# Kernel tuning notes

Measured on AMD Instinct MI355X. Metric: run time of the kernel, lower is better.

The kernel has to match this reference:

```python
import jax, jax.numpy as jnp
import numpy as np

B = 8192
IN = 1024
H = 1024


def setup_inputs() -> dict:
    key = jax.random.key(0)
    ks = jax.random.split(key, 7)
    stdv = 1.0 / np.sqrt(H)
    u = lambda k, shape: jax.random.uniform(k, shape, jnp.float32, -stdv, stdv)
    return {
        "input": jax.random.normal(ks[0], (B, IN), jnp.float32),
        "h_prev": jax.random.normal(ks[1], (B, H), jnp.float32),
        "c_prev": jax.random.normal(ks[2], (B, H), jnp.float32),
        "W_ih": u(ks[3], (4 * H, IN)),
        "b_ih": u(ks[4], (4 * H,)),
        "W_hh": u(ks[5], (4 * H, H)),
        "b_hh": u(ks[6], (4 * H,)),
    }


def reference(input, h_prev, c_prev, W_ih, b_ih, W_hh, b_hh):
    # gates: [B, 4H] = input @ W_ih^T + b_ih + h_prev @ W_hh^T + b_hh
    gates = (jnp.einsum("bi,gi->bg", input, W_ih) + b_ih
             + jnp.einsum("bh,gh->bg", h_prev, W_hh) + b_hh)
    i_in, f_in, g_in, o_in = jnp.split(gates, 4, axis=1)
    i_t = jax.nn.sigmoid(i_in)
    f_t = jax.nn.sigmoid(f_in)
    g_t = jnp.tanh(g_in)
    o_t = jax.nn.sigmoid(o_in)
    c_t = f_t * c_prev + i_t * g_t
    h_t = o_t * jnp.tanh(c_t)
    return (h_t, c_t)
```

## Files before the change

kernel.cpp:

```cpp
#include <hip/hip_runtime.h>
#include <hip/hip_bf16.h>
#include <stdint.h>


typedef __attribute__((ext_vector_type(8))) __bf16 bf16x8;
typedef __attribute__((ext_vector_type(8))) unsigned short u16x8;
typedef __attribute__((ext_vector_type(4))) float f32x4;

__device__ __forceinline__ unsigned short f2bf(float f) {
  union { float f; unsigned int u; } v; v.f = f;
  unsigned int u = v.u;
  unsigned int r = u + 0x7FFFu + ((u >> 16) & 1u);
  return (unsigned short)(r >> 16);
}

__global__ void cvt_kernel(const float* __restrict__ src,
                           unsigned short* __restrict__ dst, int n4) {
  int i = blockIdx.x * blockDim.x + threadIdx.x;
  int stride = gridDim.x * blockDim.x;
  for (; i < n4; i += stride) {
    float4 v = ((const float4*)src)[i];
    ushort4 o;
    o.x = f2bf(v.x); o.y = f2bf(v.y); o.z = f2bf(v.z); o.w = f2bf(v.w);
    ((ushort4*)dst)[i] = o;
  }
}

#define GLOAD_LDS(gp, lofs)                                                    \
  __builtin_amdgcn_global_load_lds(                                            \
      (const __attribute__((address_space(1))) void*)(gp),                     \
      (__attribute__((address_space(3))) void*)(smem_raw + (lofs)), 16, 0, 0)

__global__ void lstm_fused(const unsigned short* __restrict__ Xb,
                           const unsigned short* __restrict__ Hb,
                           const unsigned short* __restrict__ Wihb,
                           const unsigned short* __restrict__ Whhb,
                           const float* __restrict__ bih,
                           const float* __restrict__ bhh,
                           const float* __restrict__ cprev,
                           float* __restrict__ out) {
  __shared__ __align__(16) char smem_raw[32768];
  unsigned short (*sA)[64] = (unsigned short (*)[64])smem_raw;
  unsigned short (*sB)[64] = (unsigned short (*)[64])(smem_raw + 16384);
  float (*eps)[128] = (float (*)[128])smem_raw;

  const int tid = threadIdx.x;
  const int lane = tid & 63;
  const int wid = tid >> 6;
  const int wr = wid >> 1;
  const int wc = wid & 1;
  const int l15 = lane & 15;
  const int l4 = lane >> 4;

  const int m0 = blockIdx.x * 128;
  const int h0 = blockIdx.y * 32;

  const int srow = tid >> 3;
  const int scol = (tid & 7) << 3;

  f32x4 acc[4][4];
#pragma unroll
  for (int m = 0; m < 4; ++m)
#pragma unroll
    for (int n = 0; n < 4; ++n) {
      f32x4 z = {0.f, 0.f, 0.f, 0.f};
      acc[m][n] = z;
    }

  for (int k0 = 0; k0 < 2048; k0 += 64) {
    const unsigned short* As = (k0 < 1024) ? Xb : Hb;
    const unsigned short* Bs = (k0 < 1024) ? Wihb : Whhb;
    const int kk = k0 & 1023;
#pragma unroll
    for (int p = 0; p < 4; ++p) {
      const unsigned short* ga =
          As + (size_t)(m0 + p * 32 + srow) * 1024 + kk + scol;
      GLOAD_LDS(ga, p * 4096 + wid * 1024);
      const unsigned short* gb =
          Bs + (size_t)(p * 1024 + h0 + srow) * 1024 + kk + scol;
      GLOAD_LDS(gb, 16384 + p * 4096 + wid * 1024);
    }
    __syncthreads();
#pragma unroll
    for (int kk2 = 0; kk2 < 2; ++kk2) {
      bf16x8 afr[4], bfr[4];
#pragma unroll
      for (int m = 0; m < 4; ++m) {
        u16x8 t = *(const u16x8*)&sA[wr * 64 + m * 16 + l15][kk2 * 32 + l4 * 8];
        afr[m] = __builtin_bit_cast(bf16x8, t);
      }
#pragma unroll
      for (int n = 0; n < 4; ++n) {
        u16x8 t = *(const u16x8*)&sB[wc * 64 + n * 16 + l15][kk2 * 32 + l4 * 8];
        bfr[n] = __builtin_bit_cast(bf16x8, t);
      }
#pragma unroll
      for (int m = 0; m < 4; ++m)
#pragma unroll
        for (int n = 0; n < 4; ++n)
          acc[m][n] = __builtin_amdgcn_mfma_f32_16x16x32_bf16(afr[m], bfr[n],
                                                              acc[m][n], 0, 0, 0);
    }
    __syncthreads();
  }

#pragma unroll
  for (int phase = 0; phase < 2; ++phase) {
    if (wr == phase) {
#pragma unroll
      for (int m = 0; m < 4; ++m)
#pragma unroll
        for (int n = 0; n < 4; ++n)
#pragma unroll
          for (int r = 0; r < 4; ++r)
            eps[m * 16 + l4 * 4 + r][wc * 64 + n * 16 + l15] = acc[m][n][r];
    }
    __syncthreads();
#pragma unroll
    for (int it = 0; it < 8; ++it) {
      int idx = it * 256 + tid;
      int h = idx & 31;
      int r = idx >> 5;
      int gh = h0 + h;
      size_t grow = (size_t)(m0 + phase * 64 + r);
      float vi = eps[r][h]       + bih[gh]         + bhh[gh];
      float vf = eps[r][32 + h]  + bih[1024 + gh]  + bhh[1024 + gh];
      float vg = eps[r][64 + h]  + bih[2048 + gh]  + bhh[2048 + gh];
      float vo = eps[r][96 + h]  + bih[3072 + gh]  + bhh[3072 + gh];
      float si = 1.f / (1.f + __expf(-vi));
      float sf = 1.f / (1.f + __expf(-vf));
      float tg = tanhf(vg);
      float so = 1.f / (1.f + __expf(-vo));
      float cp = cprev[grow * 1024 + gh];
      float ct = sf * cp + si * tg;
      float ht = so * tanhf(ct);
      out[grow * 1024 + gh] = ht;
      out[(size_t)8388608 + grow * 1024 + gh] = ct;
    }
    __syncthreads();
  }
}

extern "C" void kernel_launch(void* const* d_in, const int* in_sizes, int n_in,
                              void* d_out, int out_size, void* d_ws, size_t ws_size,
                              hipStream_t stream) {
  const float* input  = (const float*)d_in[0];
  const float* h_prev = (const float*)d_in[1];
  const float* c_prev = (const float*)d_in[2];
  const float* W_ih   = (const float*)d_in[3];
  const float* b_ih   = (const float*)d_in[4];
  const float* W_hh   = (const float*)d_in[5];
  const float* b_hh   = (const float*)d_in[6];
  float* out = (float*)d_out;

  unsigned short* Xb   = (unsigned short*)d_ws;
  unsigned short* Hb   = Xb + (size_t)8192 * 1024;
  unsigned short* Wihb = Hb + (size_t)8192 * 1024;
  unsigned short* Whhb = Wihb + (size_t)4096 * 1024;

  cvt_kernel<<<1024, 256, 0, stream>>>(input, Xb, 8192 * 1024 / 4);
  cvt_kernel<<<1024, 256, 0, stream>>>(h_prev, Hb, 8192 * 1024 / 4);
  cvt_kernel<<<512, 256, 0, stream>>>(W_ih, Wihb, 4096 * 1024 / 4);
  cvt_kernel<<<512, 256, 0, stream>>>(W_hh, Whhb, 4096 * 1024 / 4);

  dim3 grid(64, 32);
  lstm_fused<<<grid, 256, 0, stream>>>(Xb, Hb, Wihb, Whhb, b_ih, b_hh, c_prev, out);
}
```

Measured before the change: 346.8 us.

## Rewrite LSTM GEMM with 256x64 tiles, deep LDS pipeline, merged conversion kernel

Merges the four fp32-to-bf16 conversion launches into one 2D-grid kernel that writes 8 elements per thread. The fused GEMM is restructured to 512-thread blocks computing 256x(4x64) tiles. It uses a multi-stage global_load_lds ring buffer across 128KB LDS with explicit vmcnt waits, interleaved prefetch, setprio around MFMA bursts and a swizzled block-to-tile mapping. The epilogue is reorganized to read accumulators per lane from LDS. This aims to raise data reuse and hide memory latency, at the cost of heavy LDS use that limits occupancy, and it relies on fragile manual synchronization.

Result: no change. 353.0 us (+1.8%).

```diff
diff --git a/kernel.cpp b/kernel.cpp
--- a/kernel.cpp
+++ b/kernel.cpp
@@ -9,135 +9,176 @@
 
 __device__ __forceinline__ unsigned short f2bf(float f) {
   union { float f; unsigned int u; } v; v.f = f;
-  unsigned int u = v.u;
-  unsigned int r = u + 0x7FFFu + ((u >> 16) & 1u);
+  unsigned int r = v.u + 0x7FFFu + ((v.u >> 16) & 1u);
   return (unsigned short)(r >> 16);
 }
 
-__global__ void cvt_kernel(const float* __restrict__ src,
-                           unsigned short* __restrict__ dst, int n4) {
+__global__ void cvt_all(const float* __restrict__ s0, const float* __restrict__ s1,
+                        const float* __restrict__ s2, const float* __restrict__ s3,
+                        unsigned short* __restrict__ d0, unsigned short* __restrict__ d1,
+                        unsigned short* __restrict__ d2, unsigned short* __restrict__ d3) {
+  const float* src; unsigned short* dst; int n8;
+  if (blockIdx.y == 0)      { src = s0; dst = d0; n8 = 8192 * 128; }
+  else if (blockIdx.y == 1) { src = s1; dst = d1; n8 = 8192 * 128; }
+  else if (blockIdx.y == 2) { src = s2; dst = d2; n8 = 4096 * 128; }
+  else                      { src = s3; dst = d3; n8 = 4096 * 128; }
   int i = blockIdx.x * blockDim.x + threadIdx.x;
   int stride = gridDim.x * blockDim.x;
-  for (; i < n4; i += stride) {
-    float4 v = ((const float4*)src)[i];
-    ushort4 o;
-    o.x = f2bf(v.x); o.y = f2bf(v.y); o.z = f2bf(v.z); o.w = f2bf(v.w);
-    ((ushort4*)dst)[i] = o;
+  for (; i < n8; i += stride) {
+    float4 a = ((const float4*)src)[2 * i];
+    float4 b = ((const float4*)src)[2 * i + 1];
+    u16x8 o;
+    o[0] = f2bf(a.x); o[1] = f2bf(a.y); o[2] = f2bf(a.z); o[3] = f2bf(a.w);
+    o[4] = f2bf(b.x); o[5] = f2bf(b.y); o[6] = f2bf(b.z); o[7] = f2bf(b.w);
+    *(u16x8*)&dst[(size_t)i * 8] = o;
   }
 }
 
-#define GLOAD_LDS(gp, lofs)                                                    \
-  __builtin_amdgcn_global_load_lds(                                            \
-      (const __attribute__((address_space(1))) void*)(gp),                     \
-      (__attribute__((address_space(3))) void*)(smem_raw + (lofs)), 16, 0, 0)
-
-__global__ void lstm_fused(const unsigned short* __restrict__ Xb,
-                           const unsigned short* __restrict__ Hb,
-                           const unsigned short* __restrict__ Wihb,
-                           const unsigned short* __restrict__ Whhb,
-                           const float* __restrict__ bih,
-                           const float* __restrict__ bhh,
-                           const float* __restrict__ cprev,
-                           float* __restrict__ out) {
-  __shared__ __align__(16) char smem_raw[32768];
-  unsigned short (*sA)[64] = (unsigned short (*)[64])smem_raw;
-  unsigned short (*sB)[64] = (unsigned short (*)[64])(smem_raw + 16384);
-  float (*eps)[128] = (float (*)[128])smem_raw;
+#define STAGE_HALF(G) do {                                                     \
+    const int t_ = (G) >> 2, j_ = (G) & 3;                                     \
+    const int hks_ = j_ >> 1, isB_ = j_ & 1;                                   \
+    const unsigned short* bA_; const unsigned short* bB_; int kk_;             \
+    if (t_ < 16) { bA_ = Xb; bB_ = Wihb; kk_ = t_ * 64; }                      \
+    else         { bA_ = Hb; bB_ = Whhb; kk_ = (t_ - 16) * 64; }               \
+    const int col_ = kk_ + hks_ * 32 + scol;                                   \
+    char* lb_ = smem + (((G) & 7) * 16384);                                    \
+    _Pragma("unroll")                                                          \
+    for (int r_ = 0; r_ < 2; ++r_) {                                           \
+      const int row_ = r_ * 128 + srow;                                        \
+      const unsigned short* src_ = isB_                                        \
+          ? bB_ + (size_t)((row_ >> 6) * 1024 + h0 + (row_ & 63)) * 1024 + col_\
+          : bA_ + (size_t)(m0 + row_) * 1024 + col_;                           \
+      __builtin_amdgcn_global_load_lds(                                        \
+          (const __attribute__((address_space(1))) void*)src_,                 \
+          (__attribute__((address_space(3))) void*)(lb_ + r_ * 8192 + tid * 16),\
+          16, 0, 0);                                                           \
+    }                                                                          \
+  } while (0)
+
+#define PHASE(T, B, P) do {                                                    \
+    const int ks_ = (P) >> 1, mh_ = (P) & 1;                                   \
+    const char* sa_ = smem + (4 * (B) + 2 * ks_) * 16384;                      \
+    const char* sb_ = smem + (4 * (B) + 2 * ks_ + 1) * 16384;                  \
+    bf16x8 af_[4], bf_[4];                                                     \
+    _Pragma("unroll")                                                          \
+    for (int m2 = 0; m2 < 4; ++m2) {                                           \
+      u16x8 t8 = *(const u16x8*)(sa_ +                                         \
+          ((wr * 128 + (mh_ * 4 + m2) * 16 + l15) * 64 + l4 * 16));            \
+      af_[m2] = __builtin_bit_cast(bf16x8, t8);                                \
+    }                                                                          \
+    _Pragma("unroll")                                                          \
+    for (int n_ = 0; n_ < 4; ++n_) {                                           \
+      u16x8 t8 = *(const u16x8*)(sb_ +                                         \
+          ((wc * 64 + n_ * 16 + l15) * 64 + l4 * 16));                         \
+      bf_[n_] = __builtin_bit_cast(bf16x8, t8);                                \
+    }                                                                          \
+    if (4 * (T) + 6 + (P) < 128) { STAGE_HALF(4 * (T) + 6 + (P)); }            \
+    __builtin_amdgcn_s_barrier();                                              \
+    __builtin_amdgcn_s_setprio(1);                                             \
+    _Pragma("unroll")                                                          \
+    for (int m2 = 0; m2 < 4; ++m2)                                             \
+      _Pragma("unroll")                                                        \
+      for (int n_ = 0; n_ < 4; ++n_)                                           \
+        acc[mh_ * 4 + m2][n_] = __builtin_amdgcn_mfma_f32_16x16x32_bf16(       \
+            af_[m2], bf_[n_], acc[mh_ * 4 + m2][n_], 0, 0, 0);                 \
+    __builtin_amdgcn_s_setprio(0);                                             \
+    __builtin_amdgcn_s_barrier();                                              \
+  } while (0)
+
+#define TILE(T, B) do {                                                        \
+    PHASE(T, B, 0); PHASE(T, B, 1); PHASE(T, B, 2); PHASE(T, B, 3);            \
+    if ((T) < 31) {                                                            \
+      if ((T) == 30) { asm volatile("s_waitcnt vmcnt(0)" ::: "memory"); }      \
+      else           { asm volatile("s_waitcnt vmcnt(4)" ::: "memory"); }      \
+      __builtin_amdgcn_s_barrier();                                            \
+    }                                                                          \
+  } while (0)
+
+__global__ __launch_bounds__(512, 2) void lstm_fused(
+    const unsigned short* __restrict__ Xb, const unsigned short* __restrict__ Hb,
+    const unsigned short* __restrict__ Wihb, const unsigned short* __restrict__ Whhb,
+    const float* __restrict__ bih, const float* __restrict__ bhh,
+    const float* __restrict__ cprev, float* __restrict__ out) {
+  __shared__ __align__(16) char smem[131072];
 
   const int tid = threadIdx.x;
   const int lane = tid & 63;
   const int wid = tid >> 6;
-  const int wr = wid >> 1;
-  const int wc = wid & 1;
+  const int wr = wid >> 2;
+  const int wc = wid & 3;
   const int l15 = lane & 15;
   const int l4 = lane >> 4;
 
-  const int m0 = blockIdx.x * 128;
-  const int h0 = blockIdx.y * 32;
-
-  const int srow = tid >> 3;
-  const int scol = (tid & 7) << 3;
-
-  f32x4 acc[4][4];
-#pragma unroll
-  for (int m = 0; m < 4; ++m)
+  const int bid = blockIdx.x;
+  const int tile_id = (bid & 7) * 64 + (bid >> 3);
+  const int m0 = (tile_id >> 4) * 256;
+  const int h0 = (tile_id & 15) * 64;
+
+  const int srow = tid >> 2;
+  const int scol = (tid & 3) * 8;
+
+  f32x4 acc[8][4];
+#pragma unroll
+  for (int m = 0; m < 8; ++m)
 #pragma unroll
     for (int n = 0; n < 4; ++n) {
       f32x4 z = {0.f, 0.f, 0.f, 0.f};
       acc[m][n] = z;
     }
 
-  for (int k0 = 0; k0 < 2048; k0 += 64) {
-    const unsigned short* As = (k0 < 1024) ? Xb : Hb;
-    const unsigned short* Bs = (k0 < 1024) ? Wihb : Whhb;
-    const int kk = k0 & 1023;
-#pragma unroll
-    for (int p = 0; p < 4; ++p) {
-      const unsigned short* ga =
-          As + (size_t)(m0 + p * 32 + srow) * 1024 + kk + scol;
-      GLOAD_LDS(ga, p * 4096 + wid * 1024);
-      const unsigned short* gb =
-          Bs + (size_t)(p * 1024 + h0 + srow) * 1024 + kk + scol;
-      GLOAD_LDS(gb, 16384 + p * 4096 + wid * 1024);
+  STAGE_HALF(0); STAGE_HALF(1); STAGE_HALF(2);
+  STAGE_HALF(3); STAGE_HALF(4); STAGE_HALF(5);
+  asm volatile("s_waitcnt vmcnt(4)" ::: "memory");
+  __builtin_amdgcn_s_barrier();
+
+#pragma unroll 1
+  for (int th = 0; th < 16; ++th) {
+    const int t0 = th * 2;
+    TILE(t0, 0);
+    TILE(t0 + 1, 1);
+  }
+
+  __syncthreads();
+#pragma unroll
+  for (int ph = 0; ph < 2; ++ph) {
+    if (ph) __syncthreads();
+    if (wr == ph) {
+#pragma unroll
+      for (int m = 0; m < 8; ++m)
+#pragma unroll
+        for (int n = 0; n < 4; ++n)
+          *(f32x4*)(smem + (((wc * 8 + m) * 4 + n) * 64 + lane) * 16) = acc[m][n];
     }
     __syncthreads();
 #pragma unroll
-    for (int kk2 = 0; kk2 < 2; ++kk2) {
-      bf16x8 afr[4], bfr[4];
-#pragma unroll
-      for (int m = 0; m < 4; ++m) {
-        u16x8 t = *(const u16x8*)&sA[wr * 64 + m * 16 + l15][kk2 * 32 + l4 * 8];
-        afr[m] = __builtin_bit_cast(bf16x8, t);
+    for (int q = 0; q < 4; ++q) {
+      f32x4 vg[4];
+#pragma unroll
+      for (int g = 0; g < 4; ++g)
+        vg[g] = *(const f32x4*)(smem + (((g * 8 + wid) * 4 + q) * 64 + lane) * 16);
+      const int gcol = h0 + q * 16 + l15;
+      const float b0 = bih[gcol]        + bhh[gcol];
+      const float b1 = bih[1024 + gcol] + bhh[1024 + gcol];
+      const float b2 = bih[2048 + gcol] + bhh[2048 + gcol];
+      const float b3 = bih[3072 + gcol] + bhh[3072 + gcol];
+#pragma unroll
+      for (int j = 0; j < 4; ++j) {
+        const size_t row = (size_t)(m0 + ph * 128 + wid * 16 + l4 * 4 + j);
+        const float vi = vg[0][j] + b0;
+        const float vf = vg[1][j] + b1;
+        const float vgt = vg[2][j] + b2;
+        const float vo = vg[3][j] + b3;
+        const float si = 1.f / (1.f + __expf(-vi));
+        const float sf = 1.f / (1.f + __expf(-vf));
+        const float tg = tanhf(vgt);
+        const float so = 1.f / (1.f + __expf(-vo));
+        const float cp = cprev[row * 1024 + gcol];
+        const float ct = sf * cp + si * tg;
+        const float ht = so * tanhf(ct);
+        out[row * 1024 + gcol] = ht;
+        out[8388608 + row * 1024 + gcol] = ct;
       }
-#pragma unroll
-      for (int n = 0; n < 4; ++n) {
-        u16x8 t = *(const u16x8*)&sB[wc * 64 + n * 16 + l15][kk2 * 32 + l4 * 8];
-        bfr[n] = __builtin_bit_cast(bf16x8, t);
-      }
-#pragma unroll
-      for (int m = 0; m < 4; ++m)
-#pragma unroll
-        for (int n = 0; n < 4; ++n)
-          acc[m][n] = __builtin_amdgcn_mfma_f32_16x16x32_bf16(afr[m], bfr[n],
-                                                              acc[m][n], 0, 0, 0);
     }
-    __syncthreads();
-  }
-
-#pragma unroll
-  for (int phase = 0; phase < 2; ++phase) {
-    if (wr == phase) {
-#pragma unroll
-      for (int m = 0; m < 4; ++m)
-#pragma unroll
-        for (int n = 0; n < 4; ++n)
-#pragma unroll
-          for (int r = 0; r < 4; ++r)
-            eps[m * 16 + l4 * 4 + r][wc * 64 + n * 16 + l15] = acc[m][n][r];
-    }
-    __syncthreads();
-#pragma unroll
-    for (int it = 0; it < 8; ++it) {
-      int idx = it * 256 + tid;
-      int h = idx & 31;
-      int r = idx >> 5;
-      int gh = h0 + h;
-      size_t grow = (size_t)(m0 + phase * 64 + r);
-      float vi = eps[r][h]       + bih[gh]         + bhh[gh];
-      float vf = eps[r][32 + h]  + bih[1024 + gh]  + bhh[1024 + gh];
-      float vg = eps[r][64 + h]  + bih[2048 + gh]  + bhh[2048 + gh];
-      float vo = eps[r][96 + h]  + bih[3072 + gh]  + bhh[3072 + gh];
-      float si = 1.f / (1.f + __expf(-vi));
-      float sf = 1.f / (1.f + __expf(-vf));
-      float tg = tanhf(vg);
-      float so = 1.f / (1.f + __expf(-vo));
-      float cp = cprev[grow * 1024 + gh];
-      float ct = sf * cp + si * tg;
-      float ht = so * tanhf(ct);
-      out[grow * 1024 + gh] = ht;
-      out[(size_t)8388608 + grow * 1024 + gh] = ct;
-    }
-    __syncthreads();
   }
 }
 
@@ -158,11 +199,8 @@
   unsigned short* Wihb = Hb + (size_t)8192 * 1024;
   unsigned short* Whhb = Wihb + (size_t)4096 * 1024;
 
-  cvt_kernel<<<1024, 256, 0, stream>>>(input, Xb, 8192 * 1024 / 4);
-  cvt_kernel<<<1024, 256, 0, stream>>>(h_prev, Hb, 8192 * 1024 / 4);
-  cvt_kernel<<<512, 256, 0, stream>>>(W_ih, Wihb, 4096 * 1024 / 4);
-  cvt_kernel<<<512, 256, 0, stream>>>(W_hh, Whhb, 4096 * 1024 / 4);
-
-  dim3 grid(64, 32);
-  lstm_fused<<<grid, 256, 0, stream>>>(Xb, Hb, Wihb, Whhb, b_ih, b_hh, c_prev, out);
-}
+  dim3 cgrid(1024, 4);
+  cvt_all<<<cgrid, 256, 0, stream>>>(input, h_prev, W_ih, W_hh, Xb, Hb, Wihb, Whhb);
+
+  lstm_fused<<<512, 512, 0, stream>>>(Xb, Hb, Wihb, Whhb, b_ih, b_hh, c_prev, out);
+}
```
